# Kernel tuning notes

Measured on AMD Instinct MI355X. Metric: run time of the kernel, lower is better.

## Reference

```python
import jax, jax.numpy as jnp
import numpy as np
import math

N, E, IN, OUT, H = 50000, 200000, 128, 128, 4
EPS = 1e-5
NEG_SLOPE = 0.01


def _ln(a):
    m = jnp.mean(a, axis=-1, keepdims=True)
    v = jnp.mean((a - m) ** 2, axis=-1, keepdims=True)
    return (a - m) / jnp.sqrt(v + EPS)


def setup_inputs() -> dict:
    key = jax.random.key(0)
    ks = jax.random.split(key, 24)
    glorot = lambda k, shape: jax.random.uniform(k, shape, jnp.float32,
                                                 -math.sqrt(6.0 / (shape[-2] + shape[-1])),
                                                 math.sqrt(6.0 / (shape[-2] + shape[-1])))
    lin = lambda k, fan_in, shape: jax.random.uniform(k, shape, jnp.float32,
                                                      -1.0 / math.sqrt(fan_in), 1.0 / math.sqrt(fan_in))
    inp = {
        "x": jax.random.normal(ks[0], (N, IN), jnp.float32),
        "edge_index": jax.random.randint(ks[1], (2, E), 0, N, jnp.int32),
        "edge_feature": jax.random.normal(ks[2], (E, IN), jnp.float32),
        # per-head projection matrices [H, IN, OUT]
        "Kv2v": glorot(ks[3], (H, IN, OUT)),
        "Ke2v": glorot(ks[4], (H, IN, OUT)),
        "Vv2v": glorot(ks[5], (H, IN, OUT)),
        "Ve2v": glorot(ks[6], (H, IN, OUT)),
        # per-head linear_update: [H, 2*OUT, 2*OUT]
        "lu_W": lin(ks[7], 2 * OUT, (H, 2 * OUT, 2 * OUT)),
        "lu_b": lin(ks[8], 2 * OUT, (H, 2 * OUT)),
        "ln1_g": jnp.ones((H, 2 * OUT), jnp.float32),
        "ln1_b": jnp.zeros((H, 2 * OUT), jnp.float32),
        # per-head msg_layer linear: [H, 2*OUT, OUT]
        "msg_W": lin(ks[9], 2 * OUT, (H, 2 * OUT, OUT)),
        "msg_b": lin(ks[10], 2 * OUT, (H, OUT)),
        "ln2_g": jnp.ones((H, OUT), jnp.float32),
        "ln2_b": jnp.zeros((H, OUT), jnp.float32),
        # concat projection [OUT*H, OUT]
        "cat_W": lin(ks[11], OUT * H, (OUT * H, OUT)),
        "cat_b": lin(ks[12], OUT * H, (OUT,)),
        # input projection [IN, OUT]
        "inp_W": lin(ks[13], IN, (IN, OUT)),
        "inp_b": lin(ks[14], IN, (OUT,)),
        # batchnorm affine
        "bn_g": jnp.ones((OUT,), jnp.float32),
        "bn_b": jnp.zeros((OUT,), jnp.float32),
    }
    return inp


def reference(x, edge_index, edge_feature, Kv2v, Ke2v, Vv2v, Ve2v,
              lu_W, lu_b, ln1_g, ln1_b, msg_W, msg_b, ln2_g, ln2_b,
              cat_W, cat_b, inp_W, inp_b, bn_g, bn_b):
    src, dst = edge_index[0], edge_index[1]  # j -> i
    scale = 1.0 / math.sqrt(2 * OUT)
    heads = []
    for h in range(H):  # small fixed loop over structurally distinct heads
        Kv = x @ Kv2v[h]            # [N, OUT]
        Vv = x @ Vv2v[h]
        KE = edge_feature @ Ke2v[h]  # [E, OUT]
        VE = edge_feature @ Ve2v[h]
        q_i = Kv[dst]                # [E, OUT]
        query = jnp.concatenate([q_i, q_i], axis=1)          # [E, 2*OUT]
        key_j = jnp.concatenate([Kv[src], KE], axis=1)       # [E, 2*OUT]
        alpha = query * key_j * scale
        val = jnp.concatenate([Vv[src], VE], axis=1)         # [E, 2*OUT]
        gate = jax.nn.sigmoid(_ln(alpha) * ln1_g[h] + ln1_b[h])
        m = (val @ lu_W[h] + lu_b[h]) * gate                 # [E, 2*OUT]
        m = m @ msg_W[h] + msg_b[h]                          # [E, OUT]
        m = _ln(m) * ln2_g[h] + ln2_b[h]
        m = jax.nn.leaky_relu(m, NEG_SLOPE)
        heads.append(jax.ops.segment_sum(m, dst, num_segments=N))  # [N, OUT]
    hv = jnp.concatenate(heads, axis=1)          # [N, OUT*H]
    out = hv @ cat_W + cat_b                      # [N, OUT]
    mu = jnp.mean(out, axis=0)
    var = jnp.mean((out - mu) ** 2, axis=0)      # biased, training-mode BN
    out = (out - mu) / jnp.sqrt(var + EPS) * bn_g + bn_b
    out = jax.nn.leaky_relu(out, NEG_SLOPE)
    return out + (x @ inp_W + inp_b)
```

## Files before the change

kernel.cpp:

```cpp
#include <hip/hip_runtime.h>
#include <hip/hip_bf16.h>

#define NN 50000
#define NE 200000
#define HEADS 4
#define EPSV 1e-5f
#define NEGS 0.01f

using f32x4 = __attribute__((ext_vector_type(4))) float;
using s16x8 = __attribute__((ext_vector_type(8))) short;
using bf16x8 = __attribute__((ext_vector_type(8))) __bf16;

__device__ __forceinline__ short f2bf(float f) {
    union { float f; unsigned u; } v; v.f = f;
    unsigned r = v.u + 0x7FFFu + ((v.u >> 16) & 1u);
    return (short)(r >> 16);
}
__device__ __forceinline__ float bf2f(short s) {
    union { unsigned u; float f; } v; v.u = ((unsigned)(unsigned short)s) << 16;
    return v.f;
}
__device__ __forceinline__ f32x4 mfma16(s16x8 a, s16x8 b, f32x4 c) {
    return __builtin_amdgcn_mfma_f32_16x16x32_bf16(
        __builtin_bit_cast(bf16x8, a), __builtin_bit_cast(bf16x8, b), c, 0, 0, 0);
}
__device__ __forceinline__ void gld16(const void* g, void* l) {
    __builtin_amdgcn_global_load_lds(
        (const __attribute__((address_space(1))) void*)g,
        (__attribute__((address_space(3))) void*)l, 16, 0, 0);
}
__device__ __forceinline__ void dma16(const short* src, char* dst, int w, int lane) {
    #pragma unroll
    for (int op = 0; op < 4; ++op)
        gld16(src + op * 2048 + w * 512 + lane * 8, dst + op * 4096 + w * 1024);
}

__global__ void prep_weights(const float* __restrict__ Kv2v, const float* __restrict__ Vv2v,
                             const float* __restrict__ inpW,
                             const float* __restrict__ Ke2v, const float* __restrict__ Ve2v,
                             const float* __restrict__ luW, const float* __restrict__ msgW,
                             const float* __restrict__ catW,
                             short* __restrict__ nodeW_t, short* __restrict__ imgW)
{
    int i = blockIdx.x * 256 + threadIdx.x;
    if (i < 147456) {
        int j = i >> 7, k = i & 127;
        float v;
        if (j < 512)       v = Kv2v[(j >> 7) * 16384 + k * 128 + (j & 127)];
        else if (j < 1024) v = Vv2v[((j - 512) >> 7) * 16384 + k * 128 + (j & 127)];
        else               v = inpW[k * 128 + (j - 1024)];
        nodeW_t[i] = f2bf(v);
        return;
    }
    i -= 147456;
    if (i >= 589824) return;
    int h = i / 147456;
    int r = i % 147456;
    short* img = imgW + h * 147456;
    if (r < 16384) {
        int colc = r >> 7, k = r & 127;
        img[(colc * 128 + k) ^ ((colc & 7) << 3)] = f2bf(Ke2v[h * 16384 + k * 128 + colc]);
    } else if (r < 32768) {
        int e = r - 16384; int colc = e >> 7, k = e & 127;
        img[16384 + ((colc * 128 + k) ^ ((colc & 7) << 3))] = f2bf(Ve2v[h * 16384 + k * 128 + colc]);
    } else if (r < 98304) {
        int e = r - 32768; int c = e >> 14, ec = e & 16383;
        int colc = ec >> 8, k = ec & 255; int col = c * 64 + colc;
        img[32768 + c * 16384 + ((colc * 256 + k) ^ ((colc & 7) << 3))] =
            f2bf(luW[h * 65536 + k * 256 + col]);
    } else if (r < 131072) {
        int e = r - 98304; int c = e >> 14, ec = e & 16383;
        int colc = ec >> 8, k = ec & 255; int col = c * 64 + colc;
        img[98304 + c * 16384 + ((colc * 256 + k) ^ ((colc & 7) << 3))] =
            f2bf(msgW[h * 32768 + k * 128 + col]);
    } else {
        int e = r - 131072; int colc = e >> 7, k = e & 127;
        img[131072 + ((colc * 128 + k) ^ ((colc & 7) << 3))] =
            f2bf(catW[(h * 128 + k) * 128 + colc]);
    }
}

__global__ __launch_bounds__(256, 2)
void node_proj(const float* __restrict__ x, const short* __restrict__ nodeW_t,
               short* __restrict__ Kv_all, short* __restrict__ Vv_all,
               float* __restrict__ resid)
{
    __shared__ alignas(16) short xt[64 * 128];
    const int tid = threadIdx.x;
    const int row0 = blockIdx.x * 64;
    #pragma unroll
    for (int it = 0; it < 8; ++it) {
        int idx4 = it * 256 + tid;
        int r = idx4 >> 5;
        int c = (idx4 & 31) * 4;
        float4 v = {0.f, 0.f, 0.f, 0.f};
        if (row0 + r < NN) v = *(const float4*)(x + (size_t)(row0 + r) * 128 + c);
        short4 sw; sw.x = f2bf(v.x); sw.y = f2bf(v.y); sw.z = f2bf(v.z); sw.w = f2bf(v.w);
        int byte = (r * 256 + c * 2) ^ ((r & 7) << 4);
        *(short4*)((char*)xt + byte) = sw;
    }
    __syncthreads();
    const int lane = tid & 63, w = tid >> 6;
    const int l15 = lane & 15, lg = lane >> 4;
    const int rloc = w * 16 + l15;
    s16x8 a[4];
    #pragma unroll
    for (int ks = 0; ks < 4; ++ks) {
        int byte = (rloc * 256 + (ks * 32 + lg * 8) * 2) ^ ((rloc & 7) << 4);
        a[ks] = *(const s16x8*)((const char*)xt + byte);
    }
    const int rowC = row0 + w * 16 + lg * 4;
    for (int nc = 0; nc < 18; ++nc) {
        f32x4 acc[4];
        s16x8 b[16];
        #pragma unroll
        for (int q = 0; q < 4; ++q) {
            acc[q] = (f32x4){0.f, 0.f, 0.f, 0.f};
            int j = (nc * 4 + q) * 16 + l15;
            #pragma unroll
            for (int ks = 0; ks < 4; ++ks)
                b[q * 4 + ks] = *(const s16x8*)(nodeW_t + j * 128 + ks * 32 + lg * 8);
        }
        #pragma unroll
        for (int q = 0; q < 4; ++q)
            #pragma unroll
            for (int ks = 0; ks < 4; ++ks)
                acc[q] = mfma16(a[ks], b[q * 4 + ks], acc[q]);
        #pragma unroll
        for (int q = 0; q < 4; ++q) {
            int j = (nc * 4 + q) * 16 + l15;
            #pragma unroll
            for (int r = 0; r < 4; ++r) {
                int row = rowC + r;
                if (row >= NN) continue;
                if (j < 512)       Kv_all[(size_t)row * 512 + j] = f2bf(acc[q][r]);
                else if (j < 1024) Vv_all[(size_t)row * 512 + (j - 512)] = f2bf(acc[q][r]);
                else               resid[(size_t)row * 128 + (j - 1024)] = acc[q][r];
            }
        }
    }
}

#define B128h(buf, ct, ks) \
    (*(const s16x8*)((const short*)(buf) + (((((ct) * 16 + l15) * 128) + (ks) * 32 + lg * 8) ^ ((l15 & 7) << 3))))
#define B256h(buf, ct, ks) \
    (*(const s16x8*)((const short*)(buf) + (((((ct) * 16 + l15) * 256) + (ks) * 32 + lg * 8) ^ ((l15 & 7) << 3))))
#define CB() do { __syncthreads(); char* _t = bA; bA = bB; bB = _t; } while (0)
#define PRIO1() __builtin_amdgcn_s_setprio(1)
#define PRIO0() __builtin_amdgcn_s_setprio(0)

__global__ __launch_bounds__(256, 1)
void edge_kernel(const float* __restrict__ ef, const int* __restrict__ eidx,
                 const short* __restrict__ Kv_all, const short* __restrict__ Vv_all,
                 const short* __restrict__ imgW,
                 const float* __restrict__ lu_b, const float* __restrict__ ln1_g,
                 const float* __restrict__ ln1_b, const float* __restrict__ msg_b,
                 const float* __restrict__ ln2_g, const float* __restrict__ ln2_b,
                 float* __restrict__ out1)
{
    extern __shared__ char lds[];
    char* bA = lds;
    char* bB = lds + 16384;
    const int tid = threadIdx.x;
    const int lane = tid & 63, w = tid >> 6;
    const int l15 = lane & 15, lg = lane >> 4;
    const int e0 = blockIdx.x * 64 + w * 16;
    const int rb = lg * 4;
    char* myscr = lds + 32768 + w * 12288;
    const float scale = 0.0625f;

    dma16(imgW, bB, w, lane);
    const float* efr = ef + (size_t)(e0 + l15) * 128 + lg * 8;
    s16x8 aef[4];
    #pragma unroll
    for (int ks = 0; ks < 4; ++ks) {
        float4 v0 = *(const float4*)(efr + ks * 32);
        float4 v1 = *(const float4*)(efr + ks * 32 + 4);
        s16x8 t;
        t[0] = f2bf(v0.x); t[1] = f2bf(v0.y); t[2] = f2bf(v0.z); t[3] = f2bf(v0.w);
        t[4] = f2bf(v1.x); t[5] = f2bf(v1.y); t[6] = f2bf(v1.z); t[7] = f2bf(v1.w);
        aef[ks] = t;
    }
    const int srcA = eidx[e0 + l15];
    int dstC[4];
    #pragma unroll
    for (int r = 0; r < 4; ++r) dstC[r] = eidx[NE + e0 + rb + r];
    const int gRow = lane >> 2;
    const int gChunk = lane & 3;
    const int dstG = eidx[NE + e0 + gRow];
    const int srcG = eidx[e0 + gRow];

    f32x4 outc[8];
    #pragma unroll
    for (int nt = 0; nt < 8; ++nt) outc[nt] = (f32x4){0.f, 0.f, 0.f, 0.f};
    CB();

    for (int h = 0; h < HEADS; ++h) {
        const short* hb = imgW + h * 147456;
        s16x8 qv[4], kv[4];
        #pragma unroll
        for (int j = 0; j < 4; ++j) {
            qv[j] = *(const s16x8*)(Kv_all + (size_t)dstG * 512 + h * 128 + gChunk * 32 + j * 8);
            kv[j] = *(const s16x8*)(Kv_all + (size_t)srcG * 512 + h * 128 + gChunk * 32 + j * 8);
        }

        f32x4 accK[8], accV[8];
        #pragma unroll
        for (int nt = 0; nt < 8; ++nt) { accK[nt] = (f32x4){0,0,0,0}; accV[nt] = (f32x4){0,0,0,0}; }

        dma16(hb + 8192, bB, w, lane);
        PRIO1();
        #pragma unroll
        for (int ks = 0; ks < 4; ++ks)
            #pragma unroll
            for (int ct = 0; ct < 4; ++ct)
                accK[ct] = mfma16(aef[ks], B128h(bA, ct, ks), accK[ct]);
        PRIO0();
        #pragma unroll
        for (int j = 0; j < 4; ++j) {
            int byte = gRow * 256 + ((((gChunk * 4 + j) * 16)) ^ ((gRow & 7) << 4));
            *(s16x8*)(myscr + byte) = qv[j];
            *(s16x8*)(myscr + 4096 + byte) = kv[j];
        }
        CB();

        dma16(hb + 16384, bB, w, lane);
        PRIO1();
        #pragma unroll
        for (int ks = 0; ks < 4; ++ks)
            #pragma unroll
            for (int ct = 0; ct < 4; ++ct)
                accK[4 + ct] = mfma16(aef[ks], B128h(bA, ct, ks), accK[4 + ct]);
        PRIO0();
        CB();

        dma16(hb + 24576, bB, w, lane);
        PRIO1();
        #pragma unroll
        for (int ks = 0; ks < 4; ++ks)
            #pragma unroll
            for (int ct = 0; ct < 4; ++ct)
                accV[ct] = mfma16(aef[ks], B128h(bA, ct, ks), accV[ct]);
        PRIO0();
        CB();

        dma16(hb + 32768, bB, w, lane);
        PRIO1();
        #pragma unroll
        for (int ks = 0; ks < 4; ++ks)
            #pragma unroll
            for (int ct = 0; ct < 4; ++ct)
                accV[4 + ct] = mfma16(aef[ks], B128h(bA, ct, ks), accV[4 + ct]);
        PRIO0();
        #pragma unroll
        for (int nt = 0; nt < 8; ++nt) {
            int c = nt * 16 + l15;
            #pragma unroll
            for (int r = 0; r < 4; ++r) {
                int row = rb + r;
                int byte = 8192 + ((row * 256 + c * 2) ^ ((row & 7) << 4));
                *(short*)(myscr + byte) = f2bf(accV[nt][r]);
            }
        }
        s16x8 vvr[4];
        #pragma unroll
        for (int ks = 0; ks < 4; ++ks)
            vvr[ks] = *(const s16x8*)(Vv_all + (size_t)srcA * 512 + h * 128 + ks * 32 + lg * 8);
        unsigned gpk[16][2];
        #pragma unroll
        for (int r = 0; r < 4; ++r) {
            const int i = rb + r;
            const int swz = (i & 7) << 4;
            float al[16];
            float s = 0.f, s2 = 0.f;
            #pragma unroll
            for (int nt = 0; nt < 8; ++nt) {
                int off = (i * 256 + nt * 32 + l15 * 2) ^ swz;
                float q  = bf2f(*(const short*)(myscr + off));
                float k1 = bf2f(*(const short*)(myscr + 4096 + off));
                float alo = q * k1 * scale;
                float ahi = q * accK[nt][r] * scale;
                al[nt] = alo; al[nt + 8] = ahi;
                s += alo + ahi; s2 += alo * alo + ahi * ahi;
            }
            #pragma unroll
            for (int m = 1; m < 16; m <<= 1) { s += __shfl_xor(s, m); s2 += __shfl_xor(s2, m); }
            float mean = s * (1.f / 256.f);
            float var  = s2 * (1.f / 256.f) - mean * mean;
            float rstd = rsqrtf(var + EPSV);
            #pragma unroll
            for (int i2 = 0; i2 < 16; ++i2) {
                int c = i2 * 16 + l15;
                float z = (al[i2] - mean) * rstd * ln1_g[h * 256 + c] + ln1_b[h * 256 + c];
                float g = 1.f / (1.f + __expf(-z));
                unsigned gb = (unsigned)(unsigned short)f2bf(g);
                if ((r & 1) == 0) gpk[i2][r >> 1] = gb;
                else              gpk[i2][r >> 1] |= gb << 16;
            }
        }
        CB();

        f32x4 m1[16];
        #pragma unroll
        for (int nt = 0; nt < 16; ++nt) m1[nt] = (f32x4){0, 0, 0, 0};
        #pragma unroll
        for (int c = 0; c < 8; ++c) {
            dma16(c < 7 ? hb + 32768 + (c + 1) * 8192 : hb + 98304, bB, w, lane);
            PRIO1();
            #pragma unroll
            for (int ks = 0; ks < 8; ++ks) {
                s16x8 a;
                if (ks < 4) a = vvr[ks];
                else {
                    int byte = 8192 + ((l15 * 256 + ((ks - 4) * 32 + lg * 8) * 2) ^ ((l15 & 7) << 4));
                    a = *(const s16x8*)(myscr + byte);
                }
                m1[c * 2]     = mfma16(a, B256h(bA, 0, ks), m1[c * 2]);
                m1[c * 2 + 1] = mfma16(a, B256h(bA, 1, ks), m1[c * 2 + 1]);
            }
            PRIO0();
            CB();
        }
        #pragma unroll
        for (int nt = 0; nt < 16; ++nt) {
            int c = nt * 16 + l15;
            float bias = lu_b[h * 256 + c];
            #pragma unroll
            for (int r = 0; r < 4; ++r) {
                float g = bf2f((short)((gpk[nt][r >> 1] >> ((r & 1) * 16)) & 0xFFFFu));
                int row = rb + r;
                int byte = (row * 512 + c * 2) ^ ((row & 7) << 4);
                *(short*)(myscr + byte) = f2bf((m1[nt][r] + bias) * g);
            }
        }

        f32x4 m2[8];
        #pragma unroll
        for (int nt = 0; nt < 8; ++nt) m2[nt] = (f32x4){0, 0, 0, 0};
        #pragma unroll
        for (int c = 0; c < 4; ++c) {
            dma16(c < 3 ? hb + 98304 + (c + 1) * 8192 : hb + 131072, bB, w, lane);
            PRIO1();
            #pragma unroll
            for (int ks = 0; ks < 8; ++ks) {
                int byte = (l15 * 512 + (ks * 32 + lg * 8) * 2) ^ ((l15 & 7) << 4);
                s16x8 a = *(const s16x8*)(myscr + byte);
                m2[c * 2]     = mfma16(a, B256h(bA, 0, ks), m2[c * 2]);
                m2[c * 2 + 1] = mfma16(a, B256h(bA, 1, ks), m2[c * 2 + 1]);
            }
            PRIO0();
            CB();
        }
        {
            float s[4] = {0, 0, 0, 0}, s2[4] = {0, 0, 0, 0};
            #pragma unroll
            for (int nt = 0; nt < 8; ++nt) {
                int c = nt * 16 + l15;
                float bias = msg_b[h * 128 + c];
                #pragma unroll
                for (int r = 0; r < 4; ++r) {
                    float v = m2[nt][r] + bias;
                    m2[nt][r] = v;
                    s[r] += v; s2[r] += v * v;
                }
            }
            #pragma unroll
            for (int m = 1; m < 16; m <<= 1)
                #pragma unroll
                for (int r = 0; r < 4; ++r) { s[r] += __shfl_xor(s[r], m); s2[r] += __shfl_xor(s2[r], m); }
            float mean[4], rstd[4];
            #pragma unroll
            for (int r = 0; r < 4; ++r) {
                mean[r] = s[r] * (1.f / 128.f);
                float var = s2[r] * (1.f / 128.f) - mean[r] * mean[r];
                rstd[r] = rsqrtf(var + EPSV);
            }
            #pragma unroll
            for (int nt = 0; nt < 8; ++nt) {
                int c = nt * 16 + l15;
                float g2 = ln2_g[h * 128 + c], b2 = ln2_b[h * 128 + c];
                #pragma unroll
                for (int r = 0; r < 4; ++r) {
                    float v = (m2[nt][r] - mean[r]) * rstd[r] * g2 + b2;
                    v = v > 0.f ? v : v * NEGS;
                    int row = rb + r;
                    int byte = 8192 + ((row * 256 + c * 2) ^ ((row & 7) << 4));
                    *(short*)(myscr + byte) = f2bf(v);
                }
            }
        }

        dma16(hb + 139264, bB, w, lane);
        PRIO1();
        #pragma unroll
        for (int ks = 0; ks < 4; ++ks) {
            int byte = 8192 + ((l15 * 256 + (ks * 32 + lg * 8) * 2) ^ ((l15 & 7) << 4));
            s16x8 a = *(const s16x8*)(myscr + byte);
            #pragma unroll
            for (int ct = 0; ct < 4; ++ct)
                outc[ct] = mfma16(a, B128h(bA, ct, ks), outc[ct]);
        }
        PRIO0();
        CB();

        if (h < 3) dma16(imgW + (h + 1) * 147456, bB, w, lane);
        PRIO1();
        #pragma unroll
        for (int ks = 0; ks < 4; ++ks) {
            int byte = 8192 + ((l15 * 256 + (ks * 32 + lg * 8) * 2) ^ ((l15 & 7) << 4));
            s16x8 a = *(const s16x8*)(myscr + byte);
            #pragma unroll
            for (int ct = 0; ct < 4; ++ct)
                outc[4 + ct] = mfma16(a, B128h(bA, ct, ks), outc[4 + ct]);
        }
        PRIO0();
        CB();
    }

    #pragma unroll
    for (int nt = 0; nt < 8; ++nt) {
        int c = nt * 16 + l15;
        #pragma unroll
        for (int r = 0; r < 4; ++r)
            atomicAdd(out1 + (size_t)dstC[r] * 128 + c, outc[nt][r]);
    }
}

__global__ void bn_stats(const float* __restrict__ out1, const float* __restrict__ cat_b,
                         float* __restrict__ stats)
{
    const int col = threadIdx.x;
    const int r0 = blockIdx.x * 128;
    const float cb = cat_b[col];
    float s = 0.f, s2 = 0.f;
    for (int i = 0; i < 128; ++i) {
        int row = r0 + i;
        if (row < NN) {
            float v = out1[(size_t)row * 128 + col] + cb;
            s += v; s2 += v * v;
        }
    }
    atomicAdd(stats + col, s);
    atomicAdd(stats + 128 + col, s2);
}

__global__ void finalize(const float* __restrict__ out1, const float* __restrict__ resid,
                         const float* __restrict__ stats, const float* __restrict__ cat_b,
                         const float* __restrict__ bn_g, const float* __restrict__ bn_b,
                         const float* __restrict__ inp_b, float* __restrict__ out)
{
    int i = blockIdx.x * 256 + threadIdx.x;
    if (i >= NN * 128) return;
    int col = i & 127;
    float mu = stats[col] * (1.f / NN);
    float var = stats[128 + col] * (1.f / NN) - mu * mu;
    float rstd = rsqrtf(var + EPSV);
    float v = out1[i] + cat_b[col];
    v = (v - mu) * rstd * bn_g[col] + bn_b[col];
    v = v > 0.f ? v : v * NEGS;
    out[i] = v + resid[i] + inp_b[col];
}

extern "C" void kernel_launch(void* const* d_in, const int* in_sizes, int n_in,
                              void* d_out, int out_size, void* d_ws, size_t ws_size,
                              hipStream_t stream)
{
    (void)in_sizes; (void)n_in; (void)out_size; (void)ws_size;
    const float* x     = (const float*)d_in[0];
    const int*   eidx  = (const int*)d_in[1];
    const float* ef    = (const float*)d_in[2];
    const float* Kv2v  = (const float*)d_in[3];
    const float* Ke2v  = (const float*)d_in[4];
    const float* Vv2v  = (const float*)d_in[5];
    const float* Ve2v  = (const float*)d_in[6];
    const float* lu_W  = (const float*)d_in[7];
    const float* lu_b  = (const float*)d_in[8];
    const float* ln1_g = (const float*)d_in[9];
    const float* ln1_b = (const float*)d_in[10];
    const float* msg_W = (const float*)d_in[11];
    const float* msg_b = (const float*)d_in[12];
    const float* ln2_g = (const float*)d_in[13];
    const float* ln2_b = (const float*)d_in[14];
    const float* cat_W = (const float*)d_in[15];
    const float* cat_b = (const float*)d_in[16];
    const float* inp_W = (const float*)d_in[17];
    const float* inp_b = (const float*)d_in[18];
    const float* bn_g  = (const float*)d_in[19];
    const float* bn_b  = (const float*)d_in[20];

    char* ws = (char*)d_ws;
    short* nodeW_t = (short*)(ws + 0);
    short* imgW    = (short*)(ws + 294912);
    short* Kv_all  = (short*)(ws + 1474560);
    short* Vv_all  = (short*)(ws + 52674560);
    float* resid   = (float*)(ws + 103874560);
    float* out1    = (float*)(ws + 129474560);
    float* stats   = (float*)(ws + 155074560);

    hipFuncSetAttribute((const void*)edge_kernel,
                        hipFuncAttributeMaxDynamicSharedMemorySize, 81920);

    hipMemsetAsync(out1, 0, 25600000 + 1024, stream);
    prep_weights<<<2880, 256, 0, stream>>>(Kv2v, Vv2v, inp_W, Ke2v, Ve2v, lu_W, msg_W, cat_W,
                                           nodeW_t, imgW);
    node_proj<<<782, 256, 0, stream>>>(x, nodeW_t, Kv_all, Vv_all, resid);
    edge_kernel<<<3125, 256, 81920, stream>>>(ef, eidx, Kv_all, Vv_all, imgW,
                                              lu_b, ln1_g, ln1_b, msg_b,
                                              ln2_g, ln2_b, out1);
    bn_stats<<<391, 128, 0, stream>>>(out1, cat_b, stats);
    finalize<<<25000, 256, 0, stream>>>(out1, resid, stats, cat_b, bn_g, bn_b, inp_b,
                                        (float*)d_out);
}
```

Baseline: 1.423 ms.

## Halve weight staging chunks to cut LDS and fuse gate epilogue per chunk

The edge kernel now streams weights in 8 KB chunks instead of 16 KB, which shrinks the double buffer and brings dynamic LDS down from 80 KB to 64 KB. The lu_W stage now applies bias and gate and writes each 16-column chunk as soon as it is computed, so it no longer holds 16 m1 accumulators. Both changes aim to lower LDS and register pressure so more blocks fit per CU. In exchange there are twice as many chunk iterations, each with its own __syncthreads, and less MFMA work to hide every DMA.

```diff
diff --git a/kernel.cpp b/kernel.cpp
--- a/kernel.cpp
+++ b/kernel.cpp
@@ -29,10 +29,9 @@
         (const __attribute__((address_space(1))) void*)g,
         (__attribute__((address_space(3))) void*)l, 16, 0, 0);
 }
-__device__ __forceinline__ void dma16(const short* src, char* dst, int w, int lane) {
-    #pragma unroll
-    for (int op = 0; op < 4; ++op)
-        gld16(src + op * 2048 + w * 512 + lane * 8, dst + op * 4096 + w * 1024);
+__device__ __forceinline__ void dma8(const short* src, char* dst, int w, int lane) {
+    gld16(src + w * 512 + lane * 8,        dst + w * 1024);
+    gld16(src + 2048 + w * 512 + lane * 8, dst + 4096 + w * 1024);
 }
 
 __global__ void prep_weights(const float* __restrict__ Kv2v, const float* __restrict__ Vv2v,
@@ -143,8 +142,8 @@
 
 #define B128h(buf, ct, ks) \
     (*(const s16x8*)((const short*)(buf) + (((((ct) * 16 + l15) * 128) + (ks) * 32 + lg * 8) ^ ((l15 & 7) << 3))))
-#define B256h(buf, ct, ks) \
-    (*(const s16x8*)((const short*)(buf) + (((((ct) * 16 + l15) * 256) + (ks) * 32 + lg * 8) ^ ((l15 & 7) << 3))))
+#define B256h(buf, ks) \
+    (*(const s16x8*)((const short*)(buf) + ((l15 * 256 + (ks) * 32 + lg * 8) ^ ((l15 & 7) << 3))))
 #define CB() do { __syncthreads(); char* _t = bA; bA = bB; bB = _t; } while (0)
 #define PRIO1() __builtin_amdgcn_s_setprio(1)
 #define PRIO0() __builtin_amdgcn_s_setprio(0)
@@ -160,16 +159,16 @@
 {
     extern __shared__ char lds[];
     char* bA = lds;
-    char* bB = lds + 16384;
+    char* bB = lds + 8192;
     const int tid = threadIdx.x;
     const int lane = tid & 63, w = tid >> 6;
     const int l15 = lane & 15, lg = lane >> 4;
     const int e0 = blockIdx.x * 64 + w * 16;
     const int rb = lg * 4;
-    char* myscr = lds + 32768 + w * 12288;
+    char* myscr = lds + 16384 + w * 12288;
     const float scale = 0.0625f;
 
-    dma16(imgW, bB, w, lane);
+    dma8(imgW, bB, w, lane);
     const float* efr = ef + (size_t)(e0 + l15) * 128 + lg * 8;
     s16x8 aef[4];
     #pragma unroll
@@ -207,105 +206,93 @@
         f32x4 accK[8], accV[8];
         #pragma unroll
         for (int nt = 0; nt < 8; ++nt) { accK[nt] = (f32x4){0,0,0,0}; accV[nt] = (f32x4){0,0,0,0}; }
-
-        dma16(hb + 8192, bB, w, lane);
-        PRIO1();
-        #pragma unroll
-        for (int ks = 0; ks < 4; ++ks)
-            #pragma unroll
-            for (int ct = 0; ct < 4; ++ct)
-                accK[ct] = mfma16(aef[ks], B128h(bA, ct, ks), accK[ct]);
-        PRIO0();
-        #pragma unroll
-        for (int j = 0; j < 4; ++j) {
-            int byte = gRow * 256 + ((((gChunk * 4 + j) * 16)) ^ ((gRow & 7) << 4));
-            *(s16x8*)(myscr + byte) = qv[j];
-            *(s16x8*)(myscr + 4096 + byte) = kv[j];
-        }
-        CB();
-
-        dma16(hb + 16384, bB, w, lane);
-        PRIO1();
-        #pragma unroll
-        for (int ks = 0; ks < 4; ++ks)
-            #pragma unroll
-            for (int ct = 0; ct < 4; ++ct)
-                accK[4 + ct] = mfma16(aef[ks], B128h(bA, ct, ks), accK[4 + ct]);
-        PRIO0();
-        CB();
-
-        dma16(hb + 24576, bB, w, lane);
-        PRIO1();
-        #pragma unroll
-        for (int ks = 0; ks < 4; ++ks)
-            #pragma unroll
-            for (int ct = 0; ct < 4; ++ct)
-                accV[ct] = mfma16(aef[ks], B128h(bA, ct, ks), accV[ct]);
-        PRIO0();
-        CB();
-
-        dma16(hb + 32768, bB, w, lane);
-        PRIO1();
-        #pragma unroll
-        for (int ks = 0; ks < 4; ++ks)
-            #pragma unroll
-            for (int ct = 0; ct < 4; ++ct)
-                accV[4 + ct] = mfma16(aef[ks], B128h(bA, ct, ks), accV[4 + ct]);
-        PRIO0();
-        #pragma unroll
-        for (int nt = 0; nt < 8; ++nt) {
-            int c = nt * 16 + l15;
-            #pragma unroll
-            for (int r = 0; r < 4; ++r) {
-                int row = rb + r;
-                int byte = 8192 + ((row * 256 + c * 2) ^ ((row & 7) << 4));
-                *(short*)(myscr + byte) = f2bf(accV[nt][r]);
-            }
-        }
         s16x8 vvr[4];
-        #pragma unroll
-        for (int ks = 0; ks < 4; ++ks)
-            vvr[ks] = *(const s16x8*)(Vv_all + (size_t)srcA * 512 + h * 128 + ks * 32 + lg * 8);
         unsigned gpk[16][2];
-        #pragma unroll
-        for (int r = 0; r < 4; ++r) {
-            const int i = rb + r;
-            const int swz = (i & 7) << 4;
-            float al[16];
-            float s = 0.f, s2 = 0.f;
-            #pragma unroll
-            for (int nt = 0; nt < 8; ++nt) {
-                int off = (i * 256 + nt * 32 + l15 * 2) ^ swz;
-                float q  = bf2f(*(const short*)(myscr + off));
-                float k1 = bf2f(*(const short*)(myscr + 4096 + off));
-                float alo = q * k1 * scale;
-                float ahi = q * accK[nt][r] * scale;
-                al[nt] = alo; al[nt + 8] = ahi;
-                s += alo + ahi; s2 += alo * alo + ahi * ahi;
-            }
-            #pragma unroll
-            for (int m = 1; m < 16; m <<= 1) { s += __shfl_xor(s, m); s2 += __shfl_xor(s2, m); }
-            float mean = s * (1.f / 256.f);
-            float var  = s2 * (1.f / 256.f) - mean * mean;
-            float rstd = rsqrtf(var + EPSV);
-            #pragma unroll
-            for (int i2 = 0; i2 < 16; ++i2) {
-                int c = i2 * 16 + l15;
-                float z = (al[i2] - mean) * rstd * ln1_g[h * 256 + c] + ln1_b[h * 256 + c];
-                float g = 1.f / (1.f + __expf(-z));
-                unsigned gb = (unsigned)(unsigned short)f2bf(g);
-                if ((r & 1) == 0) gpk[i2][r >> 1] = gb;
-                else              gpk[i2][r >> 1] |= gb << 16;
-            }
-        }
-        CB();
-
-        f32x4 m1[16];
-        #pragma unroll
-        for (int nt = 0; nt < 16; ++nt) m1[nt] = (f32x4){0, 0, 0, 0};
-        #pragma unroll
-        for (int c = 0; c < 8; ++c) {
-            dma16(c < 7 ? hb + 32768 + (c + 1) * 8192 : hb + 98304, bB, w, lane);
+
+        #pragma unroll
+        for (int i = 0; i < 4; ++i) {
+            dma8(hb + (i + 1) * 4096, bB, w, lane);
+            PRIO1();
+            #pragma unroll
+            for (int ks = 0; ks < 4; ++ks) {
+                accK[i * 2]     = mfma16(aef[ks], B128h(bA, 0, ks), accK[i * 2]);
+                accK[i * 2 + 1] = mfma16(aef[ks], B128h(bA, 1, ks), accK[i * 2 + 1]);
+            }
+            PRIO0();
+            if (i == 0) {
+                #pragma unroll
+                for (int j = 0; j < 4; ++j) {
+                    int byte = gRow * 256 + ((((gChunk * 4 + j) * 16)) ^ ((gRow & 7) << 4));
+                    *(s16x8*)(myscr + byte) = qv[j];
+                    *(s16x8*)(myscr + 4096 + byte) = kv[j];
+                }
+            }
+            CB();
+        }
+
+        #pragma unroll
+        for (int i = 0; i < 4; ++i) {
+            dma8(hb + (i + 5) * 4096, bB, w, lane);
+            PRIO1();
+            #pragma unroll
+            for (int ks = 0; ks < 4; ++ks) {
+                accV[i * 2]     = mfma16(aef[ks], B128h(bA, 0, ks), accV[i * 2]);
+                accV[i * 2 + 1] = mfma16(aef[ks], B128h(bA, 1, ks), accV[i * 2 + 1]);
+            }
+            PRIO0();
+            if (i == 3) {
+                #pragma unroll
+                for (int nt = 0; nt < 8; ++nt) {
+                    int c = nt * 16 + l15;
+                    #pragma unroll
+                    for (int r = 0; r < 4; ++r) {
+                        int row = rb + r;
+                        int byte = 8192 + ((row * 256 + c * 2) ^ ((row & 7) << 4));
+                        *(short*)(myscr + byte) = f2bf(accV[nt][r]);
+                    }
+                }
+                #pragma unroll
+                for (int ks = 0; ks < 4; ++ks)
+                    vvr[ks] = *(const s16x8*)(Vv_all + (size_t)srcA * 512 + h * 128 + ks * 32 + lg * 8);
+                #pragma unroll
+                for (int r = 0; r < 4; ++r) {
+                    const int i2r = rb + r;
+                    const int swz = (i2r & 7) << 4;
+                    float al[16];
+                    float s = 0.f, s2 = 0.f;
+                    #pragma unroll
+                    for (int nt = 0; nt < 8; ++nt) {
+                        int off = (i2r * 256 + nt * 32 + l15 * 2) ^ swz;
+                        float q  = bf2f(*(const short*)(myscr + off));
+                        float k1 = bf2f(*(const short*)(myscr + 4096 + off));
+                        float alo = q * k1 * scale;
+                        float ahi = q * accK[nt][r] * scale;
+                        al[nt] = alo; al[nt + 8] = ahi;
+                        s += alo + ahi; s2 += alo * alo + ahi * ahi;
+                    }
+                    #pragma unroll
+                    for (int m = 1; m < 16; m <<= 1) { s += __shfl_xor(s, m); s2 += __shfl_xor(s2, m); }
+                    float mean = s * (1.f / 256.f);
+                    float var  = s2 * (1.f / 256.f) - mean * mean;
+                    float rstd = rsqrtf(var + EPSV);
+                    #pragma unroll
+                    for (int i2 = 0; i2 < 16; ++i2) {
+                        int c = i2 * 16 + l15;
+                        float z = (al[i2] - mean) * rstd * ln1_g[h * 256 + c] + ln1_b[h * 256 + c];
+                        float g = 1.f / (1.f + __expf(-z));
+                        unsigned gb = (unsigned)(unsigned short)f2bf(g);
+                        if ((r & 1) == 0) gpk[i2][r >> 1] = gb;
+                        else              gpk[i2][r >> 1] |= gb << 16;
+                    }
+                }
+            }
+            CB();
+        }
+
+        #pragma unroll
+        for (int c = 0; c < 16; ++c) {
+            dma8(hb + (9 + c) * 4096, bB, w, lane);
+            f32x4 m1c = (f32x4){0, 0, 0, 0};
             PRIO1();
             #pragma unroll
             for (int ks = 0; ks < 8; ++ks) {
@@ -315,38 +302,35 @@
                     int byte = 8192 + ((l15 * 256 + ((ks - 4) * 32 + lg * 8) * 2) ^ ((l15 & 7) << 4));
                     a = *(const s16x8*)(myscr + byte);
                 }
-                m1[c * 2]     = mfma16(a, B256h(bA, 0, ks), m1[c * 2]);
-                m1[c * 2 + 1] = mfma16(a, B256h(bA, 1, ks), m1[c * 2 + 1]);
+                m1c = mfma16(a, B256h(bA, ks), m1c);
             }
             PRIO0();
+            {
+                int col = c * 16 + l15;
+                float bias = lu_b[h * 256 + col];
+                #pragma unroll
+                for (int r = 0; r < 4; ++r) {
+                    float g = bf2f((short)((gpk[c][r >> 1] >> ((r & 1) * 16)) & 0xFFFFu));
+                    int row = rb + r;
+                    int byte = (row * 512 + col * 2) ^ ((row & 7) << 4);
+                    *(short*)(myscr + byte) = f2bf((m1c[r] + bias) * g);
+                }
+            }
             CB();
         }
-        #pragma unroll
-        for (int nt = 0; nt < 16; ++nt) {
-            int c = nt * 16 + l15;
-            float bias = lu_b[h * 256 + c];
-            #pragma unroll
-            for (int r = 0; r < 4; ++r) {
-                float g = bf2f((short)((gpk[nt][r >> 1] >> ((r & 1) * 16)) & 0xFFFFu));
-                int row = rb + r;
-                int byte = (row * 512 + c * 2) ^ ((row & 7) << 4);
-                *(short*)(myscr + byte) = f2bf((m1[nt][r] + bias) * g);
-            }
-        }
 
         f32x4 m2[8];
         #pragma unroll
         for (int nt = 0; nt < 8; ++nt) m2[nt] = (f32x4){0, 0, 0, 0};
         #pragma unroll
-        for (int c = 0; c < 4; ++c) {
-            dma16(c < 3 ? hb + 98304 + (c + 1) * 8192 : hb + 131072, bB, w, lane);
+        for (int c = 0; c < 8; ++c) {
+            dma8(hb + (25 + c) * 4096, bB, w, lane);
             PRIO1();
             #pragma unroll
             for (int ks = 0; ks < 8; ++ks) {
                 int byte = (l15 * 512 + (ks * 32 + lg * 8) * 2) ^ ((l15 & 7) << 4);
                 s16x8 a = *(const s16x8*)(myscr + byte);
-                m2[c * 2]     = mfma16(a, B256h(bA, 0, ks), m2[c * 2]);
-                m2[c * 2 + 1] = mfma16(a, B256h(bA, 1, ks), m2[c * 2 + 1]);
+                m2[c] = mfma16(a, B256h(bA, ks), m2[c]);
             }
             PRIO0();
             CB();
@@ -390,31 +374,21 @@
             }
         }
 
-        dma16(hb + 139264, bB, w, lane);
-        PRIO1();
-        #pragma unroll
-        for (int ks = 0; ks < 4; ++ks) {
-            int byte = 8192 + ((l15 * 256 + (ks * 32 + lg * 8) * 2) ^ ((l15 & 7) << 4));
-            s16x8 a = *(const s16x8*)(myscr + byte);
-            #pragma unroll
-            for (int ct = 0; ct < 4; ++ct)
-                outc[ct] = mfma16(a, B128h(bA, ct, ks), outc[ct]);
-        }
-        PRIO0();
-        CB();
-
-        if (h < 3) dma16(imgW + (h + 1) * 147456, bB, w, lane);
-        PRIO1();
-        #pragma unroll
-        for (int ks = 0; ks < 4; ++ks) {
-            int byte = 8192 + ((l15 * 256 + (ks * 32 + lg * 8) * 2) ^ ((l15 & 7) << 4));
-            s16x8 a = *(const s16x8*)(myscr + byte);
-            #pragma unroll
-            for (int ct = 0; ct < 4; ++ct)
-                outc[4 + ct] = mfma16(a, B128h(bA, ct, ks), outc[4 + ct]);
-        }
-        PRIO0();
-        CB();
+        #pragma unroll
+        for (int c = 0; c < 4; ++c) {
+            if (c < 3)      dma8(hb + (33 + c) * 4096, bB, w, lane);
+            else if (h < 3) dma8(imgW + (h + 1) * 147456, bB, w, lane);
+            PRIO1();
+            #pragma unroll
+            for (int ks = 0; ks < 4; ++ks) {
+                int byte = 8192 + ((l15 * 256 + (ks * 32 + lg * 8) * 2) ^ ((l15 & 7) << 4));
+                s16x8 a = *(const s16x8*)(myscr + byte);
+                outc[c * 2]     = mfma16(a, B128h(bA, 0, ks), outc[c * 2]);
+                outc[c * 2 + 1] = mfma16(a, B128h(bA, 1, ks), outc[c * 2 + 1]);
+            }
+            PRIO0();
+            CB();
+        }
     }
 
     #pragma unroll
@@ -498,13 +472,13 @@
     float* stats   = (float*)(ws + 155074560);
 
     hipFuncSetAttribute((const void*)edge_kernel,
-                        hipFuncAttributeMaxDynamicSharedMemorySize, 81920);
+                        hipFuncAttributeMaxDynamicSharedMemorySize, 65536);
 
     hipMemsetAsync(out1, 0, 25600000 + 1024, stream);
     prep_weights<<<2880, 256, 0, stream>>>(Kv2v, Vv2v, inp_W, Ke2v, Ve2v, lu_W, msg_W, cat_W,
                                            nodeW_t, imgW);
     node_proj<<<782, 256, 0, stream>>>(x, nodeW_t, Kv_all, Vv_all, resid);
-    edge_kernel<<<3125, 256, 81920, stream>>>(ef, eidx, Kv_all, Vv_all, imgW,
+    edge_kernel<<<3125, 256, 65536, stream>>>(ef, eidx, Kv_all, Vv_all, imgW,
                                               lu_b, ln1_g, ln1_b, msg_b,
                                               ln2_g, ln2_b, out1);
     bn_stats<<<391, 128, 0, stream>>>(out1, cat_b, stats);
```

Result: no change. 1.435 ms (+0.8%).
